# Performance work log

Hardware: AMD Instinct MI355X
Metric: run time of the kernel (lower is better)

Reference implementation:

```python
import jax, jax.numpy as jnp
import numpy as np

B = 8192
DV = 768   # visual_input_size
DT = 768   # text_input_size
E = 8      # num_experts
D = 1024   # expert_output_size
G = 2 * D  # gate_input_size
EPS = 1e-5


def setup_inputs() -> dict:
    key = jax.random.key(0)
    ks = jax.random.split(key, 14)
    s = lambda fan_in: 1.0 / np.sqrt(fan_in)
    return {
        "visual_features": jax.random.normal(ks[0], (B, DV), dtype=jnp.float32),
        "text_features": jax.random.normal(ks[1], (B, DT), dtype=jnp.float32),
        "vis_w": jax.random.uniform(ks[2], (DV, D), jnp.float32, -s(DV), s(DV)),
        "vis_b": jax.random.uniform(ks[3], (D,), jnp.float32, -s(DV), s(DV)),
        "txt_w": jax.random.uniform(ks[4], (DT, D), jnp.float32, -s(DT), s(DT)),
        "txt_b": jax.random.uniform(ks[5], (D,), jnp.float32, -s(DT), s(DT)),
        "gate_w": jax.random.uniform(ks[6], (G, E), jnp.float32, -s(G), s(G)),
        "gate_b": jax.random.uniform(ks[7], (E,), jnp.float32, -s(G), s(G)),
        "w1": jax.random.uniform(ks[8], (E, G, D), jnp.float32, -s(G), s(G)),
        "b1": jax.random.uniform(ks[9], (E, D), jnp.float32, -s(G), s(G)),
        "w2": jax.random.uniform(ks[10], (E, D, D), jnp.float32, -s(D), s(D)),
        "b2": jax.random.uniform(ks[11], (E, D), jnp.float32, -s(D), s(D)),
        "ln_g": jnp.ones((E, D), dtype=jnp.float32),
        "ln_b": jnp.zeros((E, D), dtype=jnp.float32),
    }


def reference(visual_features, text_features, vis_w, vis_b, txt_w, txt_b,
              gate_w, gate_b, w1, b1, w2, b2, ln_g, ln_b):
    # Projections + concat -> combined features [B, 2D]
    pv = visual_features @ vis_w + vis_b
    pt = text_features @ txt_w + txt_b
    combined = jnp.concatenate([pv, pt], axis=1)

    # Gate (dropout is identity at inference)
    gate_probs = jax.nn.softmax(combined @ gate_w + gate_b, axis=1)  # [B, E]

    # All experts as batched GEMMs: [B,G] x [E,G,D] -> [B,E,D]
    h = jnp.einsum('bg,egd->bed', combined, w1) + b1
    h = jax.nn.gelu(h, approximate=False)  # torch nn.GELU default = exact erf
    h = jnp.einsum('bed,edo->beo', h, w2) + b2

    # Per-expert LayerNorm over last dim
    mu = jnp.mean(h, axis=-1, keepdims=True)
    var = jnp.mean(jnp.square(h - mu), axis=-1, keepdims=True)
    h = (h - mu) * jax.lax.rsqrt(var + EPS) * ln_g + ln_b

    # Gated reduction over experts
    return jnp.einsum('bed,be->bd', h, gate_probs)
```

## Files before the change

kernel.cpp:

```cpp
#include <hip/hip_runtime.h>
#include <hip/hip_bf16.h>
#include <math.h>

#define BM 128
#define BN 128
#define BK 64

typedef __bf16 bf16x8_t __attribute__((ext_vector_type(8)));
typedef __bf16 bf16x4_t __attribute__((ext_vector_type(4)));
typedef float f32x16_t __attribute__((ext_vector_type(16)));

static __device__ __forceinline__ float bf2f(__bf16 b) {
    unsigned short s = __builtin_bit_cast(unsigned short, b);
    unsigned int u = ((unsigned int)s) << 16;
    return __builtin_bit_cast(float, u);
}
static __device__ __forceinline__ __bf16 f2bf(float f) {
    unsigned int u = __builtin_bit_cast(unsigned int, f);
    unsigned int r = (u + 0x7fffu + ((u >> 16) & 1u)) >> 16;
    return __builtin_bit_cast(__bf16, (unsigned short)r);
}
static __device__ __forceinline__ float gelu_fast(float x) {
    const float s = x * (0.7978845608f + 0.0356774081f * x * x);
    const float e = __expf(-2.0f * s);
    return x * __builtin_amdgcn_rcpf(1.0f + e);
}

#define GLDS16(gp, lp)                                                                   \
    __builtin_amdgcn_global_load_lds((const __attribute__((address_space(1))) void*)(gp), \
                                     (__attribute__((address_space(3))) void*)(lp), 16, 0, 0)

__global__ __launch_bounds__(256) void frag_cast(const float* __restrict__ in,
                                                 __bf16* __restrict__ out,
                                                 int K, int N,
                                                 size_t inStride, size_t outStride) {
    in += (size_t)blockIdx.z * inStride;
    out += (size_t)blockIdx.z * outStride;
    __shared__ float tile[64][65];
    const int k0 = blockIdx.x * 64, n0 = blockIdx.y * 64;
    const int tid = threadIdx.x;
    const int r = tid >> 4, c4 = (tid & 15) * 4;
#pragma unroll
    for (int p = 0; p < 4; ++p) {
        const float4 v = *(const float4*)&in[(size_t)(k0 + r + p * 16) * N + n0 + c4];
        tile[r + p * 16][c4 + 0] = v.x;
        tile[r + p * 16][c4 + 1] = v.y;
        tile[r + p * 16][c4 + 2] = v.z;
        tile[r + p * 16][c4 + 3] = v.w;
    }
    __syncthreads();
    const int c = tid >> 5, nn0 = (tid & 31) * 2;
#pragma unroll
    for (int t = 0; t < 2; ++t) {
        const int nn = nn0 + t;
        bf16x8_t v;
#pragma unroll
        for (int j = 0; j < 8; ++j) v[j] = f2bf(tile[c * 8 + j][nn]);
        *(bf16x8_t*)&out[((size_t)(k0 >> 3) + c) * N * 8 + (size_t)(n0 + nn) * 8] = v;
    }
}

__global__ __launch_bounds__(256) void cast2_kernel(const float* __restrict__ a,
                                                    const float* __restrict__ b,
                                                    __bf16* __restrict__ out, int n8each) {
    const int i = blockIdx.x * 256 + threadIdx.x;
    if (i < 2 * n8each) {
        const int m = (i < n8each) ? 0 : 1;
        const int ii = i - m * n8each;
        const float* src = (m ? b : a) + (size_t)ii * 8;
        const int r = ii >> 7, c8 = ii & 127;
        const size_t dst = (size_t)m * 786432 + (size_t)(r >> 7) * 131072 +
                           (size_t)c8 * 1024 + (size_t)(r & 127) * 8;
        const float4* p = (const float4*)src;
        const float4 x = p[0], y = p[1];
        bf16x8_t v;
        v[0] = f2bf(x.x); v[1] = f2bf(x.y); v[2] = f2bf(x.z); v[3] = f2bf(x.w);
        v[4] = f2bf(y.x); v[5] = f2bf(y.y); v[6] = f2bf(y.z); v[7] = f2bf(y.w);
        *(bf16x8_t*)(out + dst) = v;
    }
}

__global__ __launch_bounds__(256) void cast_acat(const float* __restrict__ vis,
                                                 const float* __restrict__ txt,
                                                 __bf16* __restrict__ out, int total8) {
    const int i = blockIdx.x * 256 + threadIdx.x;
    if (i < total8) {
        const int r = i / 192;
        const int c8 = i - r * 192;
        const float* src = (c8 < 96) ? vis + (size_t)r * 768 + (size_t)c8 * 8
                                     : txt + (size_t)r * 768 + (size_t)(c8 - 96) * 8;
        const float4* p = (const float4*)src;
        const float4 x = p[0], y = p[1];
        bf16x8_t v;
        v[0] = f2bf(x.x); v[1] = f2bf(x.y); v[2] = f2bf(x.z); v[3] = f2bf(x.w);
        v[4] = f2bf(y.x); v[5] = f2bf(y.y); v[6] = f2bf(y.z); v[7] = f2bf(y.w);
        const size_t dst = (size_t)(r >> 7) * 196608 + (size_t)c8 * 1024 +
                           (size_t)(r & 127) * 8;
        *(bf16x8_t*)(out + dst) = v;
    }
}

#define MFMA32(a, b, c) __builtin_amdgcn_mfma_f32_32x32x16_bf16(a, b, c, 0, 0, 0)

template <int ACT, int PACK>
static __device__ __forceinline__ void gemm_core(const __bf16* __restrict__ A, int K,
                                                 const __bf16* __restrict__ Bt, int Bn,
                                                 const float* __restrict__ bias,
                                                 __bf16* __restrict__ C, int ldc,
                                                 int bm, int bn, __bf16* As) {
    const int tid = threadIdx.x;
    const int lane = tid & 63, wave = tid >> 6;
    const int wm = wave >> 1, wn = wave & 1;
    const int l = lane & 31, hi = lane >> 5;

    const __bf16* ag = A + (size_t)bm * K * 128 + (size_t)tid * 8;
    __bf16* asl = As + tid * 8;

    const __bf16* base_a = As + hi * 1024 + (wm * 64 + l) * 8;

    const size_t Bn8 = (size_t)Bn * 8;
    const __bf16* bbase = Bt + (size_t)hi * Bn8 + (size_t)(bn * BN + wn * 64 + l) * 8;
    const size_t bAdv = 8 * Bn8;

    f32x16_t acc[2][2] = {};

    const int nk = K / BK;
    for (int kt = 0; kt < nk; ++kt) {
        bf16x8_t bfr[4][2];
#pragma unroll
        for (int s = 0; s < 4; ++s) {
            bfr[s][0] = *(const bf16x8_t*)(bbase + (size_t)(2 * s) * Bn8);
            bfr[s][1] = *(const bf16x8_t*)(bbase + (size_t)(2 * s) * Bn8 + 256);
        }
        GLDS16(ag, asl);
        GLDS16(ag + 2048, asl + 2048);
        GLDS16(ag + 4096, asl + 4096);
        GLDS16(ag + 6144, asl + 6144);
        ag += 8192;
        bbase += bAdv;
        __syncthreads();
#pragma unroll
        for (int s = 0; s < 4; ++s) {
            const bf16x8_t a0 = *(const bf16x8_t*)(base_a + s * 2048);
            const bf16x8_t a1 = *(const bf16x8_t*)(base_a + s * 2048 + 256);
            acc[0][0] = MFMA32(a0, bfr[s][0], acc[0][0]);
            acc[0][1] = MFMA32(a0, bfr[s][1], acc[0][1]);
            acc[1][0] = MFMA32(a1, bfr[s][0], acc[1][0]);
            acc[1][1] = MFMA32(a1, bfr[s][1], acc[1][1]);
        }
        __syncthreads();
    }

    const int colbase = bn * BN + wn * 64 + l;
    const int rowbase = bm * BM + wm * 64 + 4 * hi;
#pragma unroll
    for (int ni = 0; ni < 2; ++ni) {
        const int col = colbase + ni * 32;
        const float bv = (PACK == 1) ? 0.0f : bias[col];
#pragma unroll
        for (int mi = 0; mi < 2; ++mi) {
#pragma unroll
            for (int v = 0; v < 16; ++v) {
                const int row = rowbase + mi * 32 + (v & 3) + 8 * (v >> 2);
                float x = acc[mi][ni][v] + bv;
                if (ACT == 1) x = gelu_fast(x);
                if (PACK == 1) {
                    C[((size_t)(row >> 3)) * (size_t)ldc * 8 + (size_t)col * 8 + (row & 7)] = f2bf(x);
                } else if (PACK == 2) {
                    C[(size_t)(row >> 7) * (size_t)ldc * 128 + (size_t)(col >> 3) * 1024 +
                      (size_t)(row & 127) * 8 + (col & 7)] = f2bf(x);
                } else {
                    C[(size_t)row * ldc + col] = f2bf(x);
                }
            }
        }
    }
}

template <int ACT, int PACK>
__global__ __launch_bounds__(256) void gemm_bt(const __bf16* __restrict__ Ab, int K, size_t strideAe,
                                               const __bf16* __restrict__ Bb, int Bn, size_t strideBe,
                                               const float* __restrict__ biasb, size_t strideBiasE,
                                               __bf16* __restrict__ Cb, int ldc, size_t strideCe) {
    __shared__ __bf16 As[BM * BK];
    gemm_core<ACT, PACK>(Ab + (size_t)blockIdx.z * strideAe, K,
                         Bb + (size_t)blockIdx.z * strideBe, Bn,
                         biasb + (size_t)blockIdx.z * strideBiasE,
                         Cb + (size_t)blockIdx.z * strideCe, ldc,
                         blockIdx.x, blockIdx.y, As);
}

__global__ __launch_bounds__(256) void gemm_premul(const __bf16* __restrict__ wbf,
                                                   const __bf16* __restrict__ w1t,
                                                   __bf16* __restrict__ w1cat) {
    __shared__ __bf16 As[BM * BK];
    const int e = blockIdx.z & 7, hf = blockIdx.z >> 3;
    gemm_core<0, 1>(wbf + (size_t)hf * 786432, 1024,
                    w1t + (size_t)e * 2048 * 1024 + (size_t)hf * 128 * 1024 * 8, 1024,
                    nullptr,
                    w1cat + (size_t)e * 1536 * 1024 + (size_t)hf * 96 * 1024 * 8, 1024,
                    blockIdx.x, blockIdx.y, As);
}

__global__ __launch_bounds__(256) void bias1_kernel(const float* __restrict__ w1,
                                                    const float* __restrict__ vis_b,
                                                    const float* __restrict__ txt_b,
                                                    const float* __restrict__ b1,
                                                    float* __restrict__ b1t) {
    const int n = blockIdx.x * 256 + threadIdx.x;
    const int e = blockIdx.y;
    const int d0 = blockIdx.z * 512;
    float acc = (blockIdx.z == 0) ? b1[(size_t)e * 1024 + n] : 0.0f;
#pragma unroll 4
    for (int d = d0; d < d0 + 512; ++d) {
        const float bv = (d < 1024) ? vis_b[d] : txt_b[d - 1024];
        acc += bv * w1[((size_t)e * 2048 + d) * 1024 + n];
    }
    atomicAdd(&b1t[(size_t)e * 1024 + n], acc);
}

__global__ __launch_bounds__(256) void gcat_kernel(const float* __restrict__ vis_w,
                                                   const float* __restrict__ txt_w,
                                                   const float* __restrict__ vis_b,
                                                   const float* __restrict__ txt_b,
                                                   const float* __restrict__ gw,
                                                   const float* __restrict__ gb,
                                                   float* __restrict__ gcat) {
    const int v = blockIdx.x, tid = threadIdx.x;
    const int lane = tid & 63, wv = tid >> 6;
    float a[8] = {0, 0, 0, 0, 0, 0, 0, 0};
    if (v < 1536) {
        const float* wr = (v < 768) ? vis_w + (size_t)v * 1024 : txt_w + (size_t)(v - 768) * 1024;
        const int dbase = (v < 768) ? 0 : 1024;
        for (int d = tid; d < 1024; d += 256) {
            const float c = wr[d];
            const float4* g4 = (const float4*)(gw + (size_t)(dbase + d) * 8);
            const float4 x = g4[0], y = g4[1];
            a[0] += c * x.x; a[1] += c * x.y; a[2] += c * x.z; a[3] += c * x.w;
            a[4] += c * y.x; a[5] += c * y.y; a[6] += c * y.z; a[7] += c * y.w;
        }
    } else {
        for (int d = tid; d < 2048; d += 256) {
            const float c = (d < 1024) ? vis_b[d] : txt_b[d - 1024];
            const float4* g4 = (const float4*)(gw + (size_t)d * 8);
            const float4 x = g4[0], y = g4[1];
            a[0] += c * x.x; a[1] += c * x.y; a[2] += c * x.z; a[3] += c * x.w;
            a[4] += c * y.x; a[5] += c * y.y; a[6] += c * y.z; a[7] += c * y.w;
        }
    }
#pragma unroll
    for (int j = 0; j < 8; ++j)
        for (int off = 32; off; off >>= 1) a[j] += __shfl_down(a[j], off, 64);
    __shared__ float red[4][8];
    if (lane == 0) {
#pragma unroll
        for (int j = 0; j < 8; ++j) red[wv][j] = a[j];
    }
    __syncthreads();
    if (tid < 8) {
        float s = red[0][tid] + red[1][tid] + red[2][tid] + red[3][tid];
        if (v == 1536) s += gb[tid];
        gcat[(size_t)v * 8 + tid] = s;
    }
}

__global__ __launch_bounds__(256) void gate_kernel(const __bf16* __restrict__ acat,
                                                   const float* __restrict__ gcat,
                                                   float* __restrict__ gate) {
    const int b = blockIdx.x, tid = threadIdx.x;
    const int lane = tid & 63, wv = tid >> 6;
    const __bf16* base = acat + (size_t)(b >> 7) * 196608 + (size_t)(b & 127) * 8;
    float a[8] = {0, 0, 0, 0, 0, 0, 0, 0};
    if (tid < 192) {
        const bf16x8_t av = *(const bf16x8_t*)(base + (size_t)tid * 1024);
#pragma unroll
        for (int jj = 0; jj < 8; ++jj) {
            const float c = bf2f(av[jj]);
            const float4* g4 = (const float4*)(gcat + (size_t)(tid * 8 + jj) * 8);
            const float4 x = g4[0], y = g4[1];
            a[0] += c * x.x; a[1] += c * x.y; a[2] += c * x.z; a[3] += c * x.w;
            a[4] += c * y.x; a[5] += c * y.y; a[6] += c * y.z; a[7] += c * y.w;
        }
    }
#pragma unroll
    for (int j = 0; j < 8; ++j)
        for (int off = 32; off; off >>= 1) a[j] += __shfl_down(a[j], off, 64);
    __shared__ float red[4][8];
    if (lane == 0) {
#pragma unroll
        for (int j = 0; j < 8; ++j) red[wv][j] = a[j];
    }
    __syncthreads();
    if (tid == 0) {
        const float* bg = gcat + 1536 * 8;
        float l[8];
        float m = -1e30f;
        for (int j = 0; j < 8; ++j) {
            l[j] = red[0][j] + red[1][j] + red[2][j] + red[3][j] + bg[j];
            m = fmaxf(m, l[j]);
        }
        float s = 0.f;
        for (int j = 0; j < 8; ++j) { l[j] = expf(l[j] - m); s += l[j]; }
        const float inv = 1.0f / s;
        for (int j = 0; j < 8; ++j) gate[(size_t)b * 8 + j] = l[j] * inv;
    }
}

__global__ __launch_bounds__(256) void ln_out_kernel(const __bf16* __restrict__ h2,
                                                     const float* __restrict__ gate,
                                                     const float* __restrict__ lng,
                                                     const float* __restrict__ lnb,
                                                     float* __restrict__ out,
                                                     int Eg, int g0, int accum) {
    const int b = blockIdx.x;
    const int tid = threadIdx.x;
    const int lane = tid & 63, wv = tid >> 6;
    const int d0 = tid * 4;
    __shared__ float sS[4], sSS[4];
    float* orow = out + (size_t)b * 1024 + d0;
    float o0, o1, o2, o3;
    if (accum) {
        const float4 p = *(const float4*)orow;
        o0 = p.x; o1 = p.y; o2 = p.z; o3 = p.w;
    } else {
        o0 = o1 = o2 = o3 = 0.f;
    }
    for (int e = 0; e < Eg; ++e) {
        const __bf16* hp = h2 + ((size_t)e * 8192 + b) * 1024 + d0;
        const bf16x4_t hv = *(const bf16x4_t*)hp;
        const float v0 = bf2f(hv[0]), v1 = bf2f(hv[1]), v2 = bf2f(hv[2]), v3 = bf2f(hv[3]);
        float s = v0 + v1 + v2 + v3;
        float ss = v0 * v0 + v1 * v1 + v2 * v2 + v3 * v3;
        for (int off = 32; off; off >>= 1) {
            s += __shfl_down(s, off, 64);
            ss += __shfl_down(ss, off, 64);
        }
        if (lane == 0) { sS[wv] = s; sSS[wv] = ss; }
        __syncthreads();
        const float S = sS[0] + sS[1] + sS[2] + sS[3];
        const float SS = sSS[0] + sSS[1] + sSS[2] + sSS[3];
        __syncthreads();
        const float mu = S * (1.0f / 1024.0f);
        const float var = SS * (1.0f / 1024.0f) - mu * mu;
        const float rstd = rsqrtf(var + 1e-5f);
        const float w = gate[(size_t)b * 8 + g0 + e];
        const float4 gg = *(const float4*)(lng + (size_t)(g0 + e) * 1024 + d0);
        const float4 bb = *(const float4*)(lnb + (size_t)(g0 + e) * 1024 + d0);
        o0 += w * ((v0 - mu) * rstd * gg.x + bb.x);
        o1 += w * ((v1 - mu) * rstd * gg.y + bb.y);
        o2 += w * ((v2 - mu) * rstd * gg.z + bb.z);
        o3 += w * ((v3 - mu) * rstd * gg.w + bb.w);
    }
    *(float4*)orow = make_float4(o0, o1, o2, o3);
}

extern "C" void kernel_launch(void* const* d_in, const int* in_sizes, int n_in,
                              void* d_out, int out_size, void* d_ws, size_t ws_size,
                              hipStream_t stream) {
    (void)in_sizes; (void)n_in; (void)out_size;
    const float* visual = (const float*)d_in[0];
    const float* text   = (const float*)d_in[1];
    const float* vis_w  = (const float*)d_in[2];
    const float* vis_b  = (const float*)d_in[3];
    const float* txt_w  = (const float*)d_in[4];
    const float* txt_b  = (const float*)d_in[5];
    const float* gate_w = (const float*)d_in[6];
    const float* gate_b = (const float*)d_in[7];
    const float* w1     = (const float*)d_in[8];
    const float* b1     = (const float*)d_in[9];
    const float* w2     = (const float*)d_in[10];
    const float* b2     = (const float*)d_in[11];
    const float* ln_g   = (const float*)d_in[12];
    const float* ln_b   = (const float*)d_in[13];
    float* out = (float*)d_out;

    const size_t B = 8192, DV = 768, D = 1024, G = 2048, E = 8, KC = 1536;

    char* ws = (char*)d_ws;
    size_t o = 0;
    auto alloc = [&](size_t bytes) { size_t r = o; o = (o + bytes + 255) & ~(size_t)255; return r; };
    const size_t off_wbf   = alloc(2 * DV * D * 2);
    const size_t off_w1cat = alloc(E * KC * D * 2);
    const size_t off_w2t   = alloc(E * D * D * 2);
    const size_t off_b1t   = alloc(E * D * 4);
    const size_t off_gcat  = alloc((KC * E + E) * 4);
    const size_t off_gate  = alloc(B * E * 4);
    const size_t off_acat  = alloc(B * KC * 2);
    const size_t fixedEnd = o;
    const size_t w1tBytes = E * G * D * 2;

    int Eg = 1;
    {
        const int cand[4] = {8, 4, 2, 1};
        for (int c = 0; c < 4; ++c) {
            size_t h2b = 2 * (size_t)cand[c] * B * D * 2;
            size_t dyn = h2b > w1tBytes ? h2b : w1tBytes;
            if (fixedEnd + dyn <= ws_size || cand[c] == 1) { Eg = cand[c]; break; }
        }
    }

    __bf16* wbf   = (__bf16*)(ws + off_wbf);
    __bf16* w1cat = (__bf16*)(ws + off_w1cat);
    __bf16* w2t   = (__bf16*)(ws + off_w2t);
    float*  b1t   = (float*)(ws + off_b1t);
    float*  gcat  = (float*)(ws + off_gcat);
    float*  gate  = (float*)(ws + off_gate);
    __bf16* acat  = (__bf16*)(ws + off_acat);
    __bf16* w1t   = (__bf16*)(ws + fixedEnd);
    __bf16* h1    = (__bf16*)(ws + fixedEnd);
    __bf16* h2    = h1 + (size_t)Eg * B * D;

    const int nw8 = (int)(DV * D / 8);
    cast2_kernel<<<(2 * nw8 + 255) / 256, 256, 0, stream>>>(vis_w, txt_w, wbf, nw8);
    const int na8 = (int)(B * KC / 8);
    cast_acat<<<(na8 + 255) / 256, 256, 0, stream>>>(visual, text, acat, na8);

    frag_cast<<<dim3(G / 64, D / 64, E), 256, 0, stream>>>(w1, w1t, (int)G, (int)D, G * D, G * D);
    frag_cast<<<dim3(D / 64, D / 64, E), 256, 0, stream>>>(w2, w2t, (int)D, (int)D, D * D, D * D);

    gemm_premul<<<dim3(768 / BM, D / BN, 16), 256, 0, stream>>>(wbf, w1t, w1cat);

    hipMemsetAsync(b1t, 0, E * D * 4, stream);
    bias1_kernel<<<dim3(4, 8, 4), 256, 0, stream>>>(w1, vis_b, txt_b, b1, b1t);
    gcat_kernel<<<1537, 256, 0, stream>>>(vis_w, txt_w, vis_b, txt_b, gate_w, gate_b, gcat);

    gate_kernel<<<(int)B, 256, 0, stream>>>(acat, gcat, gate);

    const int ng = 8 / Eg;
    for (int g = 0; g < ng; ++g) {
        const int g0 = g * Eg;
        gemm_bt<1, 2><<<dim3(B / BM, D / BN, Eg), 256, 0, stream>>>(
            acat, (int)KC, 0, w1cat + (size_t)g0 * KC * D, (int)D, KC * D,
            b1t + (size_t)g0 * D, D, h1, (int)D, B * D);
        gemm_bt<0, 0><<<dim3(B / BM, D / BN, Eg), 256, 0, stream>>>(
            h1, (int)D, B * D, w2t + (size_t)g0 * D * D, (int)D, D * D,
            b2 + (size_t)g0 * D, D, h2, (int)D, B * D);
        ln_out_kernel<<<(int)B, 256, 0, stream>>>(h2, gate, ln_g, ln_b, out, Eg, g0, g > 0 ? 1 : 0);
    }
}
```

Before: 825.7 us.

## Stage cast kernels through LDS and restructure gate kernel to 64 rows per block

```diff
diff --git a/kernel.cpp b/kernel.cpp
--- a/kernel.cpp
+++ b/kernel.cpp
@@ -62,41 +62,54 @@
 
 __global__ __launch_bounds__(256) void cast2_kernel(const float* __restrict__ a,
                                                     const float* __restrict__ b,
-                                                    __bf16* __restrict__ out, int n8each) {
-    const int i = blockIdx.x * 256 + threadIdx.x;
-    if (i < 2 * n8each) {
-        const int m = (i < n8each) ? 0 : 1;
-        const int ii = i - m * n8each;
-        const float* src = (m ? b : a) + (size_t)ii * 8;
-        const int r = ii >> 7, c8 = ii & 127;
-        const size_t dst = (size_t)m * 786432 + (size_t)(r >> 7) * 131072 +
-                           (size_t)c8 * 1024 + (size_t)(r & 127) * 8;
-        const float4* p = (const float4*)src;
-        const float4 x = p[0], y = p[1];
-        bf16x8_t v;
-        v[0] = f2bf(x.x); v[1] = f2bf(x.y); v[2] = f2bf(x.z); v[3] = f2bf(x.w);
-        v[4] = f2bf(y.x); v[5] = f2bf(y.y); v[6] = f2bf(y.z); v[7] = f2bf(y.w);
-        *(bf16x8_t*)(out + dst) = v;
+                                                    __bf16* __restrict__ out) {
+    __shared__ __align__(16) __bf16 lds[8 * 1032];
+    const int ct = blockIdx.x, mb = blockIdx.y, m = blockIdx.z, tid = threadIdx.x;
+    const int c0 = ct * 64;
+    const float* src = (m ? b : a) + (size_t)mb * 128 * 1024 + c0;
+#pragma unroll
+    for (int k = 0; k < 8; ++k) {
+        const int f = tid + k * 256;
+        const int row = f >> 4, c4 = f & 15;
+        const float4 v = *(const float4*)(src + (size_t)row * 1024 + c4 * 4);
+        __bf16* d = lds + (c4 >> 1) * 1032 + row * 8 + (c4 & 1) * 4;
+        d[0] = f2bf(v.x); d[1] = f2bf(v.y); d[2] = f2bf(v.z); d[3] = f2bf(v.w);
+    }
+    __syncthreads();
+    __bf16* dst = out + (size_t)m * 786432 + (size_t)mb * 131072 + (size_t)(c0 >> 3) * 1024;
+#pragma unroll
+    for (int k = 0; k < 4; ++k) {
+        const int g = tid + k * 256;
+        const int ch = g >> 7, row = g & 127;
+        const bf16x8_t v = *(const bf16x8_t*)(lds + ch * 1032 + row * 8);
+        *(bf16x8_t*)(dst + (size_t)ch * 1024 + row * 8) = v;
     }
 }
 
 __global__ __launch_bounds__(256) void cast_acat(const float* __restrict__ vis,
                                                  const float* __restrict__ txt,
-                                                 __bf16* __restrict__ out, int total8) {
-    const int i = blockIdx.x * 256 + threadIdx.x;
-    if (i < total8) {
-        const int r = i / 192;
-        const int c8 = i - r * 192;
-        const float* src = (c8 < 96) ? vis + (size_t)r * 768 + (size_t)c8 * 8
-                                     : txt + (size_t)r * 768 + (size_t)(c8 - 96) * 8;
-        const float4* p = (const float4*)src;
-        const float4 x = p[0], y = p[1];
-        bf16x8_t v;
-        v[0] = f2bf(x.x); v[1] = f2bf(x.y); v[2] = f2bf(x.z); v[3] = f2bf(x.w);
-        v[4] = f2bf(y.x); v[5] = f2bf(y.y); v[6] = f2bf(y.z); v[7] = f2bf(y.w);
-        const size_t dst = (size_t)(r >> 7) * 196608 + (size_t)c8 * 1024 +
-                           (size_t)(r & 127) * 8;
-        *(bf16x8_t*)(out + dst) = v;
+                                                 __bf16* __restrict__ out) {
+    __shared__ __align__(16) __bf16 lds[8 * 1032];
+    const int ct = blockIdx.x, mb = blockIdx.y, tid = threadIdx.x;
+    const int c0 = ct * 64;
+    const float* src = (c0 < 768) ? vis + (size_t)mb * 128 * 768 + c0
+                                  : txt + (size_t)mb * 128 * 768 + (c0 - 768);
+#pragma unroll
+    for (int k = 0; k < 8; ++k) {
+        const int f = tid + k * 256;
+        const int row = f >> 4, c4 = f & 15;
+        const float4 v = *(const float4*)(src + (size_t)row * 768 + c4 * 4);
+        __bf16* d = lds + (c4 >> 1) * 1032 + row * 8 + (c4 & 1) * 4;
+        d[0] = f2bf(v.x); d[1] = f2bf(v.y); d[2] = f2bf(v.z); d[3] = f2bf(v.w);
+    }
+    __syncthreads();
+    __bf16* dst = out + (size_t)mb * 196608 + (size_t)(c0 >> 3) * 1024;
+#pragma unroll
+    for (int k = 0; k < 4; ++k) {
+        const int g = tid + k * 256;
+        const int ch = g >> 7, row = g & 127;
+        const bf16x8_t v = *(const bf16x8_t*)(lds + ch * 1032 + row * 8);
+        *(bf16x8_t*)(dst + (size_t)ch * 1024 + row * 8) = v;
     }
 }
 
@@ -267,42 +280,45 @@
 __global__ __launch_bounds__(256) void gate_kernel(const __bf16* __restrict__ acat,
                                                    const float* __restrict__ gcat,
                                                    float* __restrict__ gate) {
-    const int b = blockIdx.x, tid = threadIdx.x;
+    const int bid = blockIdx.x, tid = threadIdx.x;
     const int lane = tid & 63, wv = tid >> 6;
-    const __bf16* base = acat + (size_t)(b >> 7) * 196608 + (size_t)(b & 127) * 8;
+    const int mblk = bid >> 1;
+    const int rowIn = (bid & 1) * 64 + lane;
+    const __bf16* base = acat + (size_t)mblk * 196608 + (size_t)rowIn * 8;
     float a[8] = {0, 0, 0, 0, 0, 0, 0, 0};
-    if (tid < 192) {
-        const bf16x8_t av = *(const bf16x8_t*)(base + (size_t)tid * 1024);
+    for (int k = 0; k < 48; ++k) {
+        const int c = wv + 4 * k;
+        const bf16x8_t av = *(const bf16x8_t*)(base + (size_t)c * 1024);
+        const float* g = gcat + (size_t)c * 64;
 #pragma unroll
         for (int jj = 0; jj < 8; ++jj) {
-            const float c = bf2f(av[jj]);
-            const float4* g4 = (const float4*)(gcat + (size_t)(tid * 8 + jj) * 8);
-            const float4 x = g4[0], y = g4[1];
-            a[0] += c * x.x; a[1] += c * x.y; a[2] += c * x.z; a[3] += c * x.w;
-            a[4] += c * y.x; a[5] += c * y.y; a[6] += c * y.z; a[7] += c * y.w;
-        }
-    }
-#pragma unroll
-    for (int j = 0; j < 8; ++j)
-        for (int off = 32; off; off >>= 1) a[j] += __shfl_down(a[j], off, 64);
-    __shared__ float red[4][8];
-    if (lane == 0) {
-#pragma unroll
-        for (int j = 0; j < 8; ++j) red[wv][j] = a[j];
-    }
+            const float cf = bf2f(av[jj]);
+            const float4 x = *(const float4*)(g + jj * 8);
+            const float4 y = *(const float4*)(g + jj * 8 + 4);
+            a[0] += cf * x.x; a[1] += cf * x.y; a[2] += cf * x.z; a[3] += cf * x.w;
+            a[4] += cf * y.x; a[5] += cf * y.y; a[6] += cf * y.z; a[7] += cf * y.w;
+        }
+    }
+    __shared__ float red[4][64][9];
+#pragma unroll
+    for (int j = 0; j < 8; ++j) red[wv][lane][j] = a[j];
     __syncthreads();
-    if (tid == 0) {
+    if (tid < 64) {
         const float* bg = gcat + 1536 * 8;
         float l[8];
         float m = -1e30f;
+#pragma unroll
         for (int j = 0; j < 8; ++j) {
-            l[j] = red[0][j] + red[1][j] + red[2][j] + red[3][j] + bg[j];
+            l[j] = red[0][tid][j] + red[1][tid][j] + red[2][tid][j] + red[3][tid][j] + bg[j];
             m = fmaxf(m, l[j]);
         }
         float s = 0.f;
+#pragma unroll
         for (int j = 0; j < 8; ++j) { l[j] = expf(l[j] - m); s += l[j]; }
         const float inv = 1.0f / s;
-        for (int j = 0; j < 8; ++j) gate[(size_t)b * 8 + j] = l[j] * inv;
+        const size_t r = (size_t)bid * 64 + tid;
+#pragma unroll
+        for (int j = 0; j < 8; ++j) gate[r * 8 + j] = l[j] * inv;
     }
 }
 
@@ -410,10 +426,8 @@
     __bf16* h1    = (__bf16*)(ws + fixedEnd);
     __bf16* h2    = h1 + (size_t)Eg * B * D;
 
-    const int nw8 = (int)(DV * D / 8);
-    cast2_kernel<<<(2 * nw8 + 255) / 256, 256, 0, stream>>>(vis_w, txt_w, wbf, nw8);
-    const int na8 = (int)(B * KC / 8);
-    cast_acat<<<(na8 + 255) / 256, 256, 0, stream>>>(visual, text, acat, na8);
+    cast2_kernel<<<dim3(16, 6, 2), 256, 0, stream>>>(vis_w, txt_w, wbf);
+    cast_acat<<<dim3(24, 64), 256, 0, stream>>>(visual, text, acat);
 
     frag_cast<<<dim3(G / 64, D / 64, E), 256, 0, stream>>>(w1, w1t, (int)G, (int)D, G * D, G * D);
     frag_cast<<<dim3(D / 64, D / 64, E), 256, 0, stream>>>(w2, w2t, (int)D, (int)D, D * D, D * D);
@@ -424,7 +438,7 @@
     bias1_kernel<<<dim3(4, 8, 4), 256, 0, stream>>>(w1, vis_b, txt_b, b1, b1t);
     gcat_kernel<<<1537, 256, 0, stream>>>(vis_w, txt_w, vis_b, txt_b, gate_w, gate_b, gcat);
 
-    gate_kernel<<<(int)B, 256, 0, stream>>>(acat, gcat, gate);
+    gate_kernel<<<128, 256, 0, stream>>>(acat, gcat, gate);
 
     const int ng = 8 / Eg;
     for (int g = 0; g < ng; ++g) {
```

New measurement: 772.1 us. 1.07x faster.
